# Performance work log

Hardware: AMD Instinct MI355X
Metric: run time of the kernel (lower is better)

The kernel has to match this reference:

```python
import jax, jax.numpy as jnp
import numpy as np

T, B, C = 4, 2, 128
LT, LH, LW = 8, 32, 32
NUM_HEADS = 8
HEAD_DIM = C // NUM_HEADS
THETA = 0.7
V_TH = 1.0
TAU = 2.0  # spikingjelly LIFNode default tau
N_WIN = (2, 2, 2)
TOPK = 4
EPS = 1e-5
ATAN_ALPHA = 2.0  # spikingjelly surrogate.ATan default


@jax.custom_vjp
def spike(x):
    return (x >= 0.0).astype(x.dtype)

def _spike_fwd(x):
    return spike(x), x

def _spike_bwd(x, g):
    s = (jnp.pi / 2.0) * ATAN_ALPHA * x
    return (g * (ATAN_ALPHA / 2.0) / (1.0 + s * s),)

spike.defvjp(_spike_fwd, _spike_bwd)


def lif(x_seq):
    """Multi-step LIF: v'=v+(x-v)/tau, spike at v>=V_TH, hard reset to 0 (detached)."""
    def step(v, x):
        v = v + (x - v) / TAU
        s = spike(v - V_TH)
        v = v * (1.0 - jax.lax.stop_gradient(s))  # detach_reset, v_reset=0
        return v, s
    _, s_seq = jax.lax.scan(step, jnp.zeros_like(x_seq[0]), x_seq)
    return s_seq


def bn(x, gamma, beta):
    # BatchNorm3d(track_running_stats=False) on [T*B, C, D, H, W]: batch stats per channel
    mean = x.mean(axis=(0, 1, 3, 4, 5), keepdims=True)
    var = x.var(axis=(0, 1, 3, 4, 5), keepdims=True)
    shp = (1, 1, -1, 1, 1, 1)
    return (x - mean) * jax.lax.rsqrt(var + EPS) * gamma.reshape(shp) + beta.reshape(shp)


def conv3d(x, w, pad):
    t, b = x.shape[:2]
    y = jax.lax.conv_general_dilated(
        x.reshape((t * b,) + x.shape[2:]), w,
        window_strides=(1, 1, 1), padding=[(pad, pad)] * 3,
        dimension_numbers=('NCDHW', 'OIDHW', 'NCDHW'))
    return y.reshape((t, b) + y.shape[1:])


def cdc_t(x, w):
    out = conv3d(x, w, 1)
    # central-difference temporal term: 1x1x1 conv with summed first/last temporal slices
    kd = w[:, :, 0].sum((-1, -2)) + w[:, :, 2].sum((-1, -2))  # [O, I]
    return out - THETA * jnp.einsum('oi,tbidhw->tbodhw', kd, x)


def to_wins(t):
    wt, wh, ww = N_WIN
    Tn, Bn, Cn, Lt, Lh, Lw = t.shape
    lt, lh, lw = Lt // wt, Lh // wh, Lw // ww
    t = t.reshape(Tn, Bn, Cn, wt, lt, wh, lh, ww, lw)
    t = t.transpose(0, 1, 3, 5, 7, 4, 6, 8, 2)
    return t.reshape(Tn, Bn, wt * wh * ww, lt * lh * lw, Cn)


def setup_inputs() -> dict:
    key = jax.random.key(0)
    ks = jax.random.split(key, 4)
    x = jax.random.normal(ks[0], (T, B, C, LT, LH, LW), jnp.float32)
    qw = jax.random.normal(ks[1], (C, C, 3, 3, 3), jnp.float32) / np.sqrt(C * 27)
    kw = jax.random.normal(ks[2], (C, C), jnp.float32) / np.sqrt(C)
    pw = jax.random.normal(ks[3], (C, C), jnp.float32) / np.sqrt(C)
    ones = jnp.ones((C,), jnp.float32)
    zeros = jnp.zeros((C,), jnp.float32)
    return {"x": x, "qw": qw, "q_gamma": ones, "q_beta": zeros,
            "kw": kw, "k_gamma": ones, "k_beta": zeros,
            "v_gamma": ones, "v_beta": zeros,
            "pw": pw, "p_gamma": ones, "p_beta": zeros}


def reference(x, qw, q_gamma, q_beta, kw, k_gamma, k_beta,
              v_gamma, v_beta, pw, p_gamma, p_beta):
    Tn, Bn, Cn, Lt, Lh, Lw = x.shape
    wt, wh, ww = N_WIN
    num_wins = wt * wh * ww
    lt, lh, lw = Lt // wt, Lh // wh, Lw // ww

    q_real = bn(cdc_t(x, qw), q_gamma, q_beta)
    k_real = bn(jnp.einsum('oi,tbidhw->tbodhw', kw, x), k_gamma, k_beta)

    # region-level routing from pre-spike activations
    q_region = to_wins(q_real).mean(axis=(0, 3))  # [B, W, C]
    k_region = to_wins(k_real).mean(axis=(0, 3))
    a_r = jnp.einsum('bwc,bvc->bwv', q_region, k_region) * (HEAD_DIM ** -0.5)
    k_eff = min(TOPK, num_wins)
    _, idx = jax.lax.top_k(a_r, k_eff)  # [B, W, k]

    q = lif(q_real)
    k = lif(k_real)
    v = lif(bn(x, v_gamma, v_beta))
    q_w = to_wins(q)  # [T,B,W,S,C]
    k_w = to_wins(k)
    v_w = to_wins(v)

    # gather routed windows per (batch, target window), mean-aggregate over top-k
    gather = jax.vmap(lambda src_b, idx_b: src_b[:, idx_b], in_axes=(1, 0), out_axes=1)
    k_agg = gather(k_w, idx).mean(axis=3)  # [T,B,W,S,C]
    v_agg = gather(v_w, idx).mean(axis=3)

    S = q_w.shape[3]
    q_h = q_w.reshape(Tn, Bn, num_wins, S, NUM_HEADS, HEAD_DIM)
    k_h = k_agg.reshape(Tn, Bn, num_wins, S, NUM_HEADS, HEAD_DIM)
    v_h = v_agg.reshape(Tn, Bn, num_wins, S, NUM_HEADS, HEAD_DIM)

    attn = (q_h * k_h).sum(axis=5, keepdims=True)  # [T,B,W,S,H,1]
    attn = lif(attn)
    out = (attn * v_h).reshape(Tn, Bn, num_wins, S, Cn)

    out = out.reshape(Tn, Bn, wt, wh, ww, lt, lh, lw, Cn)
    out = out.transpose(0, 1, 8, 2, 5, 3, 6, 4, 7).reshape(Tn, Bn, Cn, Lt, Lh, Lw)

    out = lif(out)
    out = bn(jnp.einsum('oi,tbidhw->tbodhw', pw, out), p_gamma, p_beta)
    return out
```

## Files before the change

### kernel.cpp

```cpp
#include <hip/hip_runtime.h>

#define TT 4
#define BB 2
#define CC 128
#define DD 8
#define HHH 32
#define WWW 32
#define PP (DD*HHH*WWW)
#define TSTRIDE (BB*CC*PP)
#define NWIN 8
#define SSS 1024
#define NHEAD 8
#define HDIM 16
#define THETA 0.7f
#define VTH 1.0f
#define NPERC (TT*BB*PP)
#define EPSf 1e-5f

typedef unsigned short ushortT;
typedef unsigned char ucharT;
typedef unsigned int uintT;
typedef _Float16 half_t;
typedef _Float16 f16x8 __attribute__((ext_vector_type(8)));
typedef float    f32x16 __attribute__((ext_vector_type(16)));

typedef const __attribute__((address_space(1))) void* as1_cvp;
typedef __attribute__((address_space(3))) void* as3_vp;

__global__ __launch_bounds__(256) void prep_wfrag(const float* __restrict__ qw,
                                                  half_t* __restrict__ wfrag) {
    int id = blockIdx.x*256 + threadIdx.x;
    if (id >= 8*27*4*64) return;
    int lane = id & 63;
    int r = id >> 6;
    int m = r & 3; r >>= 2;
    int t = r % 27;
    int kb = r / 27;
    int o   = m*32 + (lane & 31);
    int ic0 = kb*16 + (lane>>5)*8;
    size_t base = ((size_t)(id>>6))*2*64*8 + (size_t)lane*8;
    #pragma unroll
    for (int j=0;j<8;j++){
        const float* wp = qw + ((size_t)o*CC + ic0 + j)*27;
        float v = wp[t];
        if (t == 13) {
            float kd = 0.f;
            #pragma unroll
            for (int tt=0; tt<9; tt++) kd += wp[tt] + wp[18+tt];
            v -= THETA*kd;
        }
        half_t h = (half_t)v;
        half_t l = (half_t)(v - (float)h);
        wfrag[base + 0*64*8 + j] = h;
        wfrag[base + 1*64*8 + j] = l;
    }
}

__global__ __launch_bounds__(256) void prep_w1frag2(const float* __restrict__ Wk,
                                                    const float* __restrict__ Wp,
                                                    half_t* __restrict__ fragk,
                                                    half_t* __restrict__ fragp) {
    int id = blockIdx.x*256 + threadIdx.x;
    if (id >= 4096) return;
    const float* W    = (id < 2048) ? Wk : Wp;
    half_t*      frag = (id < 2048) ? fragk : fragp;
    int i2 = id & 2047;
    int lane = i2 & 63;
    int r = i2 >> 6;
    int m = r & 3;
    int kb = r >> 2;
    int o   = m*32 + (lane & 31);
    int ic0 = kb*16 + (lane>>5)*8;
    size_t base = ((size_t)(kb*4+m))*2*64*8 + (size_t)lane*8;
    #pragma unroll
    for (int j=0;j<8;j++){
        float v = W[(size_t)o*CC + ic0 + j];
        half_t h = (half_t)v;
        half_t l = (half_t)(v - (float)h);
        frag[base + 0*64*8 + j] = h;
        frag[base + 1*64*8 + j] = l;
    }
}

__global__ __launch_bounds__(256) void build_xsplit(const float* __restrict__ x,
                                                    half_t* __restrict__ xsp) {
    int id = blockIdx.x*256 + threadIdx.x;
    if (id >= 8*16*8*34*34) return;
    int wt = id % 34; int r = id/34;
    int hp = r % 34;  r /= 34;
    int dz = r % 8;   r /= 8;
    int icg = r & 15; int tb = r >> 4;
    bool inb = (hp>=1) & (hp<=32) & (wt>=1) & (wt<=32);
    half_t h8[8], l8[8];
    #pragma unroll
    for (int j=0;j<8;j++){
        float v = 0.f;
        if (inb)
            v = x[((size_t)(tb*CC + icg*8+j))*PP + (size_t)dz*1024 + (hp-1)*32 + (wt-1)];
        half_t h = (half_t)v;
        half_t l = (half_t)(v - (float)h);
        h8[j]=h; l8[j]=l;
    }
    #pragma unroll
    for (int sp=0; sp<2; sp++){
        size_t gu = (((((size_t)tb*2 + sp)*16 + icg)*8 + dz)*34 + hp)*34 + wt;
        half_t* dst = xsp + gu*8;
        const half_t* src = (sp==0)?h8:l8;
        #pragma unroll
        for (int j=0;j<8;j++) dst[j] = src[j];
    }
}

__global__ __launch_bounds__(512,2) void conv_mfma4(const half_t* __restrict__ xsp,
                                                    const half_t* __restrict__ wfrag,
                                                    float* __restrict__ y) {
    extern __shared__ half_t slab[];
    int tid  = threadIdx.x;
    int wid  = tid >> 6;
    int lane = tid & 63;
    int ln   = lane & 31;
    int half_ = lane >> 5;
    int hg = blockIdx.x;
    int dp = blockIdx.y;
    int tb = blockIdx.z;
    int H0 = hg*4, d0 = dp*2;
    int r  = wid & 3;
    int mh = wid >> 2;

    auto STAGE = [&](int kb, int bsel) {
        half_t* bufp = slab + (size_t)bsel*(3264*8);
        #pragma unroll 1
        for (int k2=0; k2<7; k2++) {
            int u = tid + (k2<<9);
            if (u < 3264) {
                int sp  = (u >= 1632) ? 1 : 0;
                int r1  = u - sp*1632;
                int icg = (r1 >= 816) ? 1 : 0;
                int p2  = r1 - icg*816;
                int dzs = p2/204; int r3 = p2 - dzs*204;
                int hp  = r3/34;  int wt = r3 - hp*34;
                int dd  = d0 - 1 + dzs;
                const half_t* src = ((unsigned)dd < 8u)
                    ? &xsp[((((((size_t)tb*2 + sp)*16 + (kb*2+icg))*8 + dd)*34 + (H0+hp))*34 + wt)*8]
                    : &xsp[(size_t)ln*8];
                __builtin_amdgcn_global_load_lds((as1_cvp)src,
                    (as3_vp)(bufp + (size_t)u*8), 16, 0, 0);
            }
        }
    };

    f32x16 accA[2][2], accB[2][2];
    #pragma unroll
    for (int dt=0;dt<2;dt++)
        #pragma unroll
        for (int mm=0;mm<2;mm++)
            #pragma unroll
            for (int i=0;i<16;i++){ accA[dt][mm][i]=0.f; accB[dt][mm][i]=0.f; }

    f16x8 ca[2][2];
    #pragma unroll
    for (int mm=0;mm<2;mm++)
        #pragma unroll
        for (int sp=0;sp<2;sp++)
            ca[mm][sp] = *(const f16x8*)&wfrag[((((size_t)0*4 + (mh*2+mm))*2+sp)*64 + lane)*8];

    asm volatile("" ::: "memory");
    STAGE(0,0);
    STAGE(1,1);
    asm volatile("" ::: "memory");

    auto KBODY = [&](int kk, f32x16 (&acc)[2][2]) {
        if (kk == 0) {
            if (wid < 3) asm volatile("s_waitcnt vmcnt(7)" ::: "memory");
            else         asm volatile("s_waitcnt vmcnt(6)" ::: "memory");
        } else {
            asm volatile("s_waitcnt vmcnt(63)" ::: "memory");
        }
        __builtin_amdgcn_s_barrier();
        asm volatile("" ::: "memory");
        const half_t* bufp = slab + (size_t)(kk&1)*(3264*8);

        f16x8 cbC[2][2], cbN[2][2];
        #pragma unroll
        for (int dt=0; dt<2; dt++){
            int unitb = dt*204 + r*34 + ln;
            #pragma unroll
            for (int sp=0; sp<2; sp++)
                cbC[dt][sp] = *(const f16x8*)&bufp[(size_t)((sp*2+half_)*816 + unitb)*8];
        }

        #pragma unroll 1
        for (int t=0; t<27; t++) {
            int t2 = (t<26)? t+1 : 26;
            int dz2=t2/9; int rr2=t2-dz2*9; int dh2=rr2/3; int dw2=rr2-dh2*3;
            #pragma unroll
            for (int dt=0; dt<2; dt++){
                int unitb = (dt + dz2)*204 + (r+dh2)*34 + (ln+dw2);
                #pragma unroll
                for (int sp=0; sp<2; sp++)
                    cbN[dt][sp] = *(const f16x8*)&bufp[(size_t)((sp*2+half_)*816 + unitb)*8];
            }
            f16x8 na[2][2];
            int nt  = (t<26)? t+1 : 0;
            int nkb = (t<26)? kk  : ((kk<7)? kk+1 : kk);
            #pragma unroll
            for (int mm=0;mm<2;mm++)
                #pragma unroll
                for (int sp=0;sp<2;sp++)
                    na[mm][sp] = *(const f16x8*)&wfrag[((((size_t)(nkb*27+nt)*4+(mh*2+mm))*2+sp)*64 + lane)*8];
            #pragma unroll
            for (int dt=0;dt<2;dt++)
                #pragma unroll
                for (int mm=0;mm<2;mm++) acc[dt][mm] = __builtin_amdgcn_mfma_f32_32x32x16_f16(ca[mm][0], cbC[dt][0], acc[dt][mm],0,0,0);
            #pragma unroll
            for (int dt=0;dt<2;dt++)
                #pragma unroll
                for (int mm=0;mm<2;mm++) acc[dt][mm] = __builtin_amdgcn_mfma_f32_32x32x16_f16(ca[mm][0], cbC[dt][1], acc[dt][mm],0,0,0);
            #pragma unroll
            for (int dt=0;dt<2;dt++)
                #pragma unroll
                for (int mm=0;mm<2;mm++) acc[dt][mm] = __builtin_amdgcn_mfma_f32_32x32x16_f16(ca[mm][1], cbC[dt][0], acc[dt][mm],0,0,0);
            #pragma unroll
            for (int dt=0;dt<2;dt++)
                #pragma unroll
                for (int sp=0;sp<2;sp++) cbC[dt][sp] = cbN[dt][sp];
            #pragma unroll
            for (int mm=0;mm<2;mm++)
                #pragma unroll
                for (int sp=0;sp<2;sp++) ca[mm][sp] = na[mm][sp];
        }
        asm volatile("" ::: "memory");
        __builtin_amdgcn_s_barrier();
        asm volatile("" ::: "memory");
        if (kk < 6) STAGE(kk+2, kk&1);
    };

    #pragma unroll 1
    for (int kk=0; kk<4; kk++) KBODY(kk, accA);
    #pragma unroll 1
    for (int kk=4; kk<8; kk++) KBODY(kk, accB);

    int h = H0 + r;
    #pragma unroll
    for (int dt=0; dt<2; dt++) {
        int d = d0 + dt;
        #pragma unroll
        for (int mm=0; mm<2; mm++) {
            #pragma unroll
            for (int reg=0; reg<16; reg++) {
                int row = (reg&3) + 8*(reg>>2) + 4*half_;
                int o = (mh*2+mm)*32 + row;
                y[((size_t)tb*CC + o)*PP + d*1024 + h*32 + ln]
                    = accA[dt][mm][reg] + accB[dt][mm][reg];
            }
        }
    }
}

__global__ __launch_bounds__(256) void kgemm_mfma(const half_t* __restrict__ xsp,
                                                  const half_t* __restrict__ wk,
                                                  float* __restrict__ y) {
    int tid  = threadIdx.x;
    int wid  = tid >> 6;
    int lane = tid & 63;
    int ln   = lane & 31;
    int half_ = lane >> 5;
    int hg = blockIdx.x, d = blockIdx.y, tb = blockIdx.z;
    int h = hg*4 + wid;

    f32x16 acc[4];
    #pragma unroll
    for (int m=0;m<4;m++)
        #pragma unroll
        for (int i=0;i<16;i++) acc[m][i] = 0.f;

    #pragma unroll 2
    for (int kb=0; kb<8; kb++) {
        f16x8 b[2];
        #pragma unroll
        for (int sp=0; sp<2; sp++) {
            size_t gu = (((((size_t)tb*2 + sp)*16 + (kb*2+half_))*8 + d)*34 + (h+1))*34 + (ln+1);
            b[sp] = *(const f16x8*)&xsp[gu*8];
        }
        #pragma unroll
        for (int m=0; m<4; m++) {
            const half_t* wb = wk + ((size_t)(kb*4+m))*2*64*8 + (size_t)lane*8;
            f16x8 a0 = *(const f16x8*)&wb[0*64*8];
            f16x8 a1 = *(const f16x8*)&wb[1*64*8];
            acc[m] = __builtin_amdgcn_mfma_f32_32x32x16_f16(a0, b[0], acc[m],0,0,0);
            acc[m] = __builtin_amdgcn_mfma_f32_32x32x16_f16(a0, b[1], acc[m],0,0,0);
            acc[m] = __builtin_amdgcn_mfma_f32_32x32x16_f16(a1, b[0], acc[m],0,0,0);
        }
    }
    #pragma unroll
    for (int m=0; m<4; m++) {
        #pragma unroll
        for (int reg=0; reg<16; reg++) {
            int row = (reg&3) + 8*(reg>>2) + 4*half_;
            int o = m*32 + row;
            y[((size_t)tb*CC + o)*PP + d*1024 + h*32 + ln] = acc[m][reg];
        }
    }
}

__global__ __launch_bounds__(256) void pgemm_mfma(const ushortT* __restrict__ spkb,
                                                  const half_t* __restrict__ wp,
                                                  float* __restrict__ y) {
    int tid  = threadIdx.x;
    int wid  = tid >> 6;
    int lane = tid & 63;
    int ln   = lane & 31;
    int half_ = lane >> 5;
    int hg = blockIdx.x, d = blockIdx.y, tb = blockIdx.z;
    int h = hg*4 + wid;
    int p = d*1024 + h*32 + ln;

    f32x16 acc[4];
    #pragma unroll
    for (int m=0;m<4;m++)
        #pragma unroll
        for (int i=0;i<16;i++) acc[m][i] = 0.f;

    #pragma unroll 2
    for (int kb=0; kb<8; kb++) {
        f16x8 b = *(const f16x8*)&spkb[(((size_t)tb*16 + (kb*2+half_))*PP + p)*8];
        #pragma unroll
        for (int m=0; m<4; m++) {
            const half_t* wb = wp + ((size_t)(kb*4+m))*2*64*8 + (size_t)lane*8;
            f16x8 a0 = *(const f16x8*)&wb[0*64*8];
            f16x8 a1 = *(const f16x8*)&wb[1*64*8];
            acc[m] = __builtin_amdgcn_mfma_f32_32x32x16_f16(a0, b, acc[m],0,0,0);
            acc[m] = __builtin_amdgcn_mfma_f32_32x32x16_f16(a1, b, acc[m],0,0,0);
        }
    }
    #pragma unroll
    for (int m=0; m<4; m++) {
        #pragma unroll
        for (int reg=0; reg<16; reg++) {
            int row = (reg&3) + 8*(reg>>2) + 4*half_;
            int o = m*32 + row;
            y[((size_t)tb*CC + o)*PP + p] = acc[m][reg];
        }
    }
}

__global__ __launch_bounds__(128) void win_stats(const float* __restrict__ q,
        const float* __restrict__ k, const float* __restrict__ x,
        float* __restrict__ rsum, float* __restrict__ rsq) {
    int blk = blockIdx.x;
    int src = blk >> 11;
    int r   = blk & 2047;
    const float* base = (src==0) ? q : ((src==1) ? k : x);
    int c  = r & 127;
    int wi = (r >> 7) & 7;
    int b  = r >> 10;
    int wd = wi>>2, wh = (wi>>1)&1, ww = wi&1;
    int tid = threadIdx.x;
    float s=0.f, s2=0.f;
    for (int t=0;t<TT;t++){
        const float* p = base + ((size_t)(t*BB+b)*CC + c)*PP;
        for (int si=tid; si<SSS; si+=128){
            int ld = si>>8, lh=(si>>4)&15, lw=si&15;
            float v = p[((wd*4+ld)<<10) + ((wh*16+lh)<<5) + (ww*16+lw)];
            s += v; s2 += v*v;
        }
    }
    __shared__ float ls[128], ls2[128];
    ls[tid]=s; ls2[tid]=s2; __syncthreads();
    for (int off=64;off>0;off>>=1){
        if(tid<off){ ls[tid]+=ls[tid+off]; ls2[tid]+=ls2[tid+off]; }
        __syncthreads();
    }
    if (tid==0){ rsum[blk]=ls[0]; rsq[blk]=ls2[0]; }
}

__global__ __launch_bounds__(384) void route_fin(const float* __restrict__ rsum,
        const float* __restrict__ rsq,
        const float* __restrict__ qg, const float* __restrict__ qb,
        const float* __restrict__ kg, const float* __restrict__ kb,
        float* __restrict__ stats, int* __restrict__ idxout) {
    __shared__ float qn[16*128], kn[16*128], ar[16*8];
    __shared__ float csum[384], csq[384];
    int tid = threadIdx.x;
    {
        int src = tid >> 7, c = tid & 127;
        float s=0.f, s2=0.f;
        for (int bw=0; bw<16; bw++){
            int idx = src*2048 + bw*128 + c;
            s  += rsum[idx];
            s2 += rsq[idx];
        }
        stats[src*256 + c]       = s;
        stats[src*256 + 128 + c] = s2;
        csum[tid]=s; csq[tid]=s2;
    }
    __syncthreads();
    for (int e=tid; e<16*128; e+=384){
        int c = e&127;
        float qm = csum[c]*(1.f/NPERC);
        float qv = csq[c]*(1.f/NPERC) - qm*qm;
        float qr = rsqrtf(qv + EPSf);
        qn[e] = (rsum[e]*(1.f/(TT*SSS)) - qm)*qr*qg[c] + qb[c];
        float km = csum[128+c]*(1.f/NPERC);
        float kv = csq[128+c]*(1.f/NPERC) - km*km;
        float kr = rsqrtf(kv + EPSf);
        kn[e] = (rsum[2048+e]*(1.f/(TT*SSS)) - km)*kr*kg[c] + kb[c];
    }
    __syncthreads();
    if (tid < 128){
        int b = tid>>6, w=(tid>>3)&7, v=tid&7;
        float s=0.f;
        for (int c=0;c<128;c++) s += qn[(b*8+w)*128+c]*kn[(b*8+v)*128+c];
        ar[(b*8+w)*8+v] = s * 0.25f;
    }
    __syncthreads();
    if (tid < 16){
        const float* row = &ar[tid*8];
        bool used[8] = {false,false,false,false,false,false,false,false};
        for (int j=0;j<4;j++){
            int best=0; float bv=-3.0e38f;
            for (int v=0; v<8; v++){
                if (!used[v] && row[v] > bv){ bv=row[v]; best=v; }
            }
            used[best]=true;
            idxout[tid*4+j]=best;
        }
    }
}

__global__ __launch_bounds__(256) void lif_bn_win3(const float* __restrict__ qin,
        const float* __restrict__ kin, const float* __restrict__ xin,
        ucharT* __restrict__ qs, ucharT* __restrict__ ks, ucharT* __restrict__ vs,
        const float* __restrict__ stats,
        const float* __restrict__ qg, const float* __restrict__ qb,
        const float* __restrict__ kg, const float* __restrict__ kb,
        const float* __restrict__ vg, const float* __restrict__ vb) {
    int src = blockIdx.y;
    const float* in  = (src==0) ? qin : ((src==1) ? kin : xin);
    ucharT*      spk = (src==0) ? qs  : ((src==1) ? ks  : vs);
    const float* gamma = (src==0) ? qg : ((src==1) ? kg : vg);
    const float* beta  = (src==0) ? qb : ((src==1) ? kb : vb);
    int e4 = blockIdx.x*256 + threadIdx.x;
    if (e4 >= BB*CC*PP/4) return;
    int e = e4*4;
    int p = e & (PP-1);
    int c = (e >> 13) & 127;
    int b = e >> 20;
    float mean = stats[src*256 + c]*(1.f/NPERC);
    float var  = stats[src*256 + 128 + c]*(1.f/NPERC) - mean*mean;
    float sc = rsqrtf(var+EPSf)*gamma[c];
    float sh = beta[c] - mean*sc;
    int d = p>>10, h=(p>>5)&31, w=p&31;
    int wi = ((d>>2)*2 + (h>>4))*2 + (w>>4);
    int si = (((d&3)<<4) + (h&15))*16 + (w&15);
    size_t widx = ((size_t)(b*NWIN+wi)*CC + c)*SSS + si;
    float v[4] = {0.f,0.f,0.f,0.f};
    #pragma unroll
    for (int t=0;t<TT;t++){
        float4 raw = *(const float4*)&in[(size_t)t*TSTRIDE + e];
        float xs[4] = {raw.x, raw.y, raw.z, raw.w};
        uintT pack = 0;
        #pragma unroll
        for (int i=0;i<4;i++){
            float xn = xs[i]*sc + sh;
            v[i] = (v[i]+xn)*0.5f;
            float s = (v[i]>=VTH)?1.f:0.f;
            pack |= (v[i]>=VTH ? 1u : 0u) << (8*i);
            v[i] *= (1.f - s);
        }
        *(uintT*)&spk[(size_t)t*TSTRIDE + widx] = pack;
    }
}

__global__ __launch_bounds__(256) void attn_lif(const ucharT* __restrict__ qspk,
        const ucharT* __restrict__ kspk, const ucharT* __restrict__ vspk,
        const int* __restrict__ idx, ushortT* __restrict__ spkb) {
    int id = blockIdx.x*256 + threadIdx.x;
    int ddq = id & 3;
    int s4  = (id>>2) & 255;
    int hh  = (id>>10) & 7;
    int wi  = (id>>13) & 7;
    int b   = id>>16;
    int bw  = b*NWIN+wi;
    int s0  = s4*4;
    int dd0 = ddq*4;
    size_t qbase = ((size_t)bw*CC + hh*HDIM + dd0)*SSS + s0;
    size_t sbase[4];
    #pragma unroll
    for (int j=0;j<4;j++){
        int srcw = idx[bw*4+j];
        sbase[j] = ((size_t)(b*NWIN+srcw)*CC + hh*HDIM + dd0)*SSS + s0;
    }
    int wd = wi>>2, wh = (wi>>1)&1, ww = wi&1;
    int d3 = wd*4 + (s0>>8), h3 = wh*16 + ((s0>>4)&15), w3 = ww*16 + (s0&15);
    int p0 = (d3<<10) + (h3<<5) + w3;
    int icg  = hh*2 + (ddq>>1);
    int slot = (ddq&1)*4;

    float v[4] = {0.f,0.f,0.f,0.f};
    float v2[4][4];
    #pragma unroll
    for (int i=0;i<4;i++)
        #pragma unroll
        for (int si=0;si<4;si++) v2[i][si]=0.f;

    #pragma unroll 1
    for (int t=0;t<TT;t++){
        size_t toff = (size_t)t*TSTRIDE;
        uintT km[4] = {0,0,0,0}, vm[4] = {0,0,0,0};
        #pragma unroll
        for (int j=0;j<4;j++){
            const ucharT* kp = kspk+toff+sbase[j];
            const ucharT* vp = vspk+toff+sbase[j];
            #pragma unroll
            for (int i=0; i<4; i++){
                km[i] += *(const uintT*)&kp[(size_t)i*SSS];
                vm[i] += *(const uintT*)&vp[(size_t)i*SSS];
            }
        }
        const ucharT* qp = qspk+toff+qbase;
        uintT atti = 0;
        #pragma unroll
        for (int i=0;i<4;i++){
            uintT q4 = *(const uintT*)&qp[(size_t)i*SSS];
            uintT tq = (q4 + 0x7F7F7F7Fu) & 0x80808080u;
            uintT mask = tq - (tq >> 7);
            atti += km[i] & mask;
        }
        atti += (uintT)__shfl_xor((int)atti, 1);
        atti += (uintT)__shfl_xor((int)atti, 2);
        int tb2 = t*BB + b;
        size_t obase = (((size_t)tb2*16 + icg)*PP + p0)*8 + slot;
        #pragma unroll
        for (int si=0; si<4; si++){
            float att = (float)((atti >> (8*si)) & 255u) * 0.25f;
            v[si] = (v[si]+att)*0.5f;
            float sp = (v[si]>=VTH)?1.f:0.f;
            v[si] *= (1.f-sp);
            float spq = sp*0.25f;
            uintT lo=0, hi=0;
            #pragma unroll
            for (int i=0;i<4;i++){
                float ov = spq*(float)((vm[i] >> (8*si)) & 255u);
                v2[i][si] = (v2[i][si]+ov)*0.5f;
                float s2 = (v2[i][si]>=VTH)?1.f:0.f;
                v2[i][si] *= (1.f-s2);
                uintT bs = (s2 != 0.f) ? 0x3C00u : 0u;
                if (i<2) lo |= bs << (16*i); else hi |= bs << (16*(i-2));
            }
            uint2 pk; pk.x = lo; pk.y = hi;
            *(uint2*)&spkb[obase + (size_t)si*8] = pk;
        }
    }
}

__global__ __launch_bounds__(256) void pstats_part(const float* __restrict__ xin,
        float* __restrict__ part_sum, float* __restrict__ part_sq) {
    int blk = blockIdx.x;
    int c = blk & 127, tb = blk >> 7;
    int tid = threadIdx.x;
    const float* p = xin + ((size_t)tb*CC + c)*PP;
    float s=0.f, s2=0.f;
    for (int i=tid; i<PP; i+=256){ float v=p[i]; s+=v; s2+=v*v; }
    __shared__ float ls[256], ls2[256];
    ls[tid]=s; ls2[tid]=s2; __syncthreads();
    for (int off=128; off>0; off>>=1){
        if (tid<off){ ls[tid]+=ls[tid+off]; ls2[tid]+=ls2[tid+off]; }
        __syncthreads();
    }
    if (tid==0){ part_sum[blk]=ls[0]; part_sq[blk]=ls2[0]; }
}

__global__ __launch_bounds__(256) void bn_apply(const float* __restrict__ xin,
        float* __restrict__ yout,
        const float* __restrict__ part_sum, const float* __restrict__ part_sq,
        const float* __restrict__ gamma, const float* __restrict__ beta) {
    size_t i = (size_t)blockIdx.x*256 + threadIdx.x;
    if (i >= (size_t)TT*BB*CC*PP) return;
    int c = (int)((i>>13)&127);
    float s=0.f, s2=0.f;
    #pragma unroll
    for (int tb=0; tb<8; tb++){
        s  += part_sum[tb*128+c];
        s2 += part_sq[tb*128+c];
    }
    float mean = s*(1.f/NPERC);
    float var  = s2*(1.f/NPERC) - mean*mean;
    float sc = rsqrtf(var+EPSf)*gamma[c];
    float sh = beta[c] - mean*sc;
    yout[i] = xin[i]*sc + sh;
}

extern "C" void kernel_launch(void* const* d_in, const int* in_sizes, int n_in,
                              void* d_out, int out_size, void* d_ws, size_t ws_size,
                              hipStream_t stream) {
    const float* x  = (const float*)d_in[0];
    const float* qw = (const float*)d_in[1];
    const float* qg = (const float*)d_in[2];
    const float* qb = (const float*)d_in[3];
    const float* kw = (const float*)d_in[4];
    const float* kg = (const float*)d_in[5];
    const float* kb = (const float*)d_in[6];
    const float* vg = (const float*)d_in[7];
    const float* vb = (const float*)d_in[8];
    const float* pw = (const float*)d_in[9];
    const float* pg = (const float*)d_in[10];
    const float* pb = (const float*)d_in[11];
    float* out = (float*)d_out;
    float* ws  = (float*)d_ws;

    const size_t NEL = (size_t)TT*TSTRIDE;
    float* qconv = ws;
    half_t* xsp  = (half_t*)(ws + 2*NEL);
    const size_t KCONV_OFF = 2*NEL + 10747904;
    float* kconv = ws + KCONV_OFF;
    float* wf_base = ws + KCONV_OFF + NEL;
    half_t* wfrag  = (half_t*)wf_base;
    half_t* wkfrag = (half_t*)(wf_base + 442368);
    half_t* wpfrag = (half_t*)(wf_base + 442368 + 16384 + 442368);
    float* stats = ws + 5*NEL;
    float* rsum = stats + 1024;
    float* rsq  = rsum + 6144;
    float* ppart_sum = rsq + 6144;
    float* ppart_sq  = ppart_sum + 1024;
    int*   idxp = (int*)(ppart_sq + 1024);

    ucharT* qspk = (ucharT*)(ws + 2*NEL);
    ucharT* kspk = (ucharT*)(ws + 2*NEL) + 8388608;
    ucharT* vspk = (ucharT*)(ws + 2*NEL) + 16777216;
    ushortT* spkb  = (ushortT*)ws;
    float*  pconv  = ws + KCONV_OFF;

    prep_wfrag<<<216,256,0,stream>>>(qw, wfrag);
    prep_w1frag2<<<16,256,0,stream>>>(kw, pw, wkfrag, wpfrag);
    build_xsplit<<<4624,256,0,stream>>>(x, xsp);
    {
        static bool attr_set = false;
        const int shmem = 2*3264*8*(int)sizeof(half_t);
        if (!attr_set) {
            hipFuncSetAttribute((const void*)conv_mfma4,
                                hipFuncAttributeMaxDynamicSharedMemorySize, shmem);
            attr_set = true;
        }
        dim3 cg(8,4,8);
        conv_mfma4<<<cg,512,shmem,stream>>>(xsp, wfrag, qconv);
    }
    {
        dim3 gg(8,8,8);
        kgemm_mfma<<<gg,256,0,stream>>>(xsp, wkfrag, kconv);
    }
    win_stats<<<6144,128,0,stream>>>(qconv, kconv, x, rsum, rsq);
    route_fin<<<1,384,0,stream>>>(rsum, rsq, qg,qb,kg,kb, stats, idxp);
    {
        dim3 lg(2048,3);
        lif_bn_win3<<<lg,256,0,stream>>>(qconv,kconv,x,
                                         qspk,kspk,vspk,
                                         stats, qg,qb,kg,kb,vg,vb);
    }
    attn_lif<<<512,256,0,stream>>>(qspk,kspk,vspk,idxp,spkb);
    {
        dim3 gg(8,8,8);
        pgemm_mfma<<<gg,256,0,stream>>>(spkb, wpfrag, pconv);
    }
    pstats_part<<<1024,256,0,stream>>>(pconv, ppart_sum, ppart_sq);
    bn_apply<<<32768,256,0,stream>>>(pconv, out, ppart_sum, ppart_sq, pg, pb);
}
```

Before: 385.8 us.

## Fuse prep kernels, merge k-GEMM into conv, fold BN stats into p-GEMM

Combines the three preparation kernels into one launch and runs the 1x1 k-projection GEMM inside the 3x3x3 conv kernel after its main loop. The projection GEMM now accumulates per-channel sum and sum-of-squares through shared-memory and global atomics, which removes the separate statistics pass; the accumulators are zeroed inside attn_lif. bn_apply reads the totals directly and uses float4 vector loads and stores. This cuts launch count and one full read of the projection output, at the cost of atomic contention, a longer conv kernel tail, and atomic-order nondeterminism in the BN statistics.

```diff
diff --git a/kernel.cpp b/kernel.cpp
--- a/kernel.cpp
+++ b/kernel.cpp
@@ -27,93 +27,97 @@
 typedef const __attribute__((address_space(1))) void* as1_cvp;
 typedef __attribute__((address_space(3))) void* as3_vp;
 
-__global__ __launch_bounds__(256) void prep_wfrag(const float* __restrict__ qw,
-                                                  half_t* __restrict__ wfrag) {
-    int id = blockIdx.x*256 + threadIdx.x;
-    if (id >= 8*27*4*64) return;
-    int lane = id & 63;
-    int r = id >> 6;
-    int m = r & 3; r >>= 2;
-    int t = r % 27;
-    int kb = r / 27;
-    int o   = m*32 + (lane & 31);
-    int ic0 = kb*16 + (lane>>5)*8;
-    size_t base = ((size_t)(id>>6))*2*64*8 + (size_t)lane*8;
-    #pragma unroll
-    for (int j=0;j<8;j++){
-        const float* wp = qw + ((size_t)o*CC + ic0 + j)*27;
-        float v = wp[t];
-        if (t == 13) {
-            float kd = 0.f;
-            #pragma unroll
-            for (int tt=0; tt<9; tt++) kd += wp[tt] + wp[18+tt];
-            v -= THETA*kd;
-        }
-        half_t h = (half_t)v;
-        half_t l = (half_t)(v - (float)h);
-        wfrag[base + 0*64*8 + j] = h;
-        wfrag[base + 1*64*8 + j] = l;
-    }
-}
-
-__global__ __launch_bounds__(256) void prep_w1frag2(const float* __restrict__ Wk,
-                                                    const float* __restrict__ Wp,
-                                                    half_t* __restrict__ fragk,
-                                                    half_t* __restrict__ fragp) {
-    int id = blockIdx.x*256 + threadIdx.x;
-    if (id >= 4096) return;
-    const float* W    = (id < 2048) ? Wk : Wp;
-    half_t*      frag = (id < 2048) ? fragk : fragp;
-    int i2 = id & 2047;
-    int lane = i2 & 63;
-    int r = i2 >> 6;
-    int m = r & 3;
-    int kb = r >> 2;
-    int o   = m*32 + (lane & 31);
-    int ic0 = kb*16 + (lane>>5)*8;
-    size_t base = ((size_t)(kb*4+m))*2*64*8 + (size_t)lane*8;
-    #pragma unroll
-    for (int j=0;j<8;j++){
-        float v = W[(size_t)o*CC + ic0 + j];
-        half_t h = (half_t)v;
-        half_t l = (half_t)(v - (float)h);
-        frag[base + 0*64*8 + j] = h;
-        frag[base + 1*64*8 + j] = l;
-    }
-}
-
-__global__ __launch_bounds__(256) void build_xsplit(const float* __restrict__ x,
-                                                    half_t* __restrict__ xsp) {
-    int id = blockIdx.x*256 + threadIdx.x;
-    if (id >= 8*16*8*34*34) return;
-    int wt = id % 34; int r = id/34;
-    int hp = r % 34;  r /= 34;
-    int dz = r % 8;   r /= 8;
-    int icg = r & 15; int tb = r >> 4;
-    bool inb = (hp>=1) & (hp<=32) & (wt>=1) & (wt<=32);
-    half_t h8[8], l8[8];
-    #pragma unroll
-    for (int j=0;j<8;j++){
-        float v = 0.f;
-        if (inb)
-            v = x[((size_t)(tb*CC + icg*8+j))*PP + (size_t)dz*1024 + (hp-1)*32 + (wt-1)];
-        half_t h = (half_t)v;
-        half_t l = (half_t)(v - (float)h);
-        h8[j]=h; l8[j]=l;
-    }
-    #pragma unroll
-    for (int sp=0; sp<2; sp++){
-        size_t gu = (((((size_t)tb*2 + sp)*16 + icg)*8 + dz)*34 + hp)*34 + wt;
-        half_t* dst = xsp + gu*8;
-        const half_t* src = (sp==0)?h8:l8;
-        #pragma unroll
-        for (int j=0;j<8;j++) dst[j] = src[j];
+__global__ __launch_bounds__(256) void prep_all(const float* __restrict__ qw,
+                                                const float* __restrict__ Wk,
+                                                const float* __restrict__ Wp,
+                                                const float* __restrict__ x,
+                                                half_t* __restrict__ wfrag,
+                                                half_t* __restrict__ fragk,
+                                                half_t* __restrict__ fragp,
+                                                half_t* __restrict__ xsp) {
+    int bid = blockIdx.x;
+    int tid = threadIdx.x;
+    if (bid < 216) {
+        int id = bid*256 + tid;
+        if (id >= 8*27*4*64) return;
+        int lane = id & 63;
+        int r = id >> 6;
+        int m = r & 3; r >>= 2;
+        int t = r % 27;
+        int kb = r / 27;
+        int o   = m*32 + (lane & 31);
+        int ic0 = kb*16 + (lane>>5)*8;
+        size_t base = ((size_t)(id>>6))*2*64*8 + (size_t)lane*8;
+        #pragma unroll
+        for (int j=0;j<8;j++){
+            const float* wp = qw + ((size_t)o*CC + ic0 + j)*27;
+            float v = wp[t];
+            if (t == 13) {
+                float kd = 0.f;
+                #pragma unroll
+                for (int tt=0; tt<9; tt++) kd += wp[tt] + wp[18+tt];
+                v -= THETA*kd;
+            }
+            half_t h = (half_t)v;
+            half_t l = (half_t)(v - (float)h);
+            wfrag[base + 0*64*8 + j] = h;
+            wfrag[base + 1*64*8 + j] = l;
+        }
+    } else if (bid < 232) {
+        int id = (bid-216)*256 + tid;
+        if (id >= 4096) return;
+        const float* W    = (id < 2048) ? Wk : Wp;
+        half_t*      frag = (id < 2048) ? fragk : fragp;
+        int i2 = id & 2047;
+        int lane = i2 & 63;
+        int r = i2 >> 6;
+        int m = r & 3;
+        int kb = r >> 2;
+        int o   = m*32 + (lane & 31);
+        int ic0 = kb*16 + (lane>>5)*8;
+        size_t base = ((size_t)(kb*4+m))*2*64*8 + (size_t)lane*8;
+        #pragma unroll
+        for (int j=0;j<8;j++){
+            float v = W[(size_t)o*CC + ic0 + j];
+            half_t h = (half_t)v;
+            half_t l = (half_t)(v - (float)h);
+            frag[base + 0*64*8 + j] = h;
+            frag[base + 1*64*8 + j] = l;
+        }
+    } else {
+        int id = (bid-232)*256 + tid;
+        if (id >= 8*16*8*34*34) return;
+        int wt = id % 34; int r = id/34;
+        int hp = r % 34;  r /= 34;
+        int dz = r % 8;   r /= 8;
+        int icg = r & 15; int tb = r >> 4;
+        bool inb = (hp>=1) & (hp<=32) & (wt>=1) & (wt<=32);
+        half_t h8[8], l8[8];
+        #pragma unroll
+        for (int j=0;j<8;j++){
+            float v = 0.f;
+            if (inb)
+                v = x[((size_t)(tb*CC + icg*8+j))*PP + (size_t)dz*1024 + (hp-1)*32 + (wt-1)];
+            half_t h = (half_t)v;
+            half_t l = (half_t)(v - (float)h);
+            h8[j]=h; l8[j]=l;
+        }
+        #pragma unroll
+        for (int sp=0; sp<2; sp++){
+            size_t gu = (((((size_t)tb*2 + sp)*16 + icg)*8 + dz)*34 + hp)*34 + wt;
+            half_t* dst = xsp + gu*8;
+            const half_t* src = (sp==0)?h8:l8;
+            #pragma unroll
+            for (int j=0;j<8;j++) dst[j] = src[j];
+        }
     }
 }
 
 __global__ __launch_bounds__(512,2) void conv_mfma4(const half_t* __restrict__ xsp,
                                                     const half_t* __restrict__ wfrag,
-                                                    float* __restrict__ y) {
+                                                    const half_t* __restrict__ wk,
+                                                    float* __restrict__ y,
+                                                    float* __restrict__ yk) {
     extern __shared__ half_t slab[];
     int tid  = threadIdx.x;
     int wid  = tid >> 6;
@@ -240,72 +244,69 @@
     #pragma unroll 1
     for (int kk=4; kk<8; kk++) KBODY(kk, accB);
 
-    int h = H0 + r;
-    #pragma unroll
-    for (int dt=0; dt<2; dt++) {
-        int d = d0 + dt;
-        #pragma unroll
-        for (int mm=0; mm<2; mm++) {
+    {
+        int h = H0 + r;
+        #pragma unroll
+        for (int dt=0; dt<2; dt++) {
+            int d = d0 + dt;
+            #pragma unroll
+            for (int mm=0; mm<2; mm++) {
+                #pragma unroll
+                for (int reg=0; reg<16; reg++) {
+                    int row = (reg&3) + 8*(reg>>2) + 4*half_;
+                    int o = (mh*2+mm)*32 + row;
+                    y[((size_t)tb*CC + o)*PP + d*1024 + h*32 + ln]
+                        = accA[dt][mm][reg] + accB[dt][mm][reg];
+                }
+            }
+        }
+    }
+
+    {
+        int d = d0 + (wid >> 2);
+        int h = H0 + (wid & 3);
+        f32x16 kacc[4];
+        #pragma unroll
+        for (int m=0;m<4;m++)
+            #pragma unroll
+            for (int i=0;i<16;i++) kacc[m][i] = 0.f;
+
+        #pragma unroll 2
+        for (int kb=0; kb<8; kb++) {
+            f16x8 b[2];
+            #pragma unroll
+            for (int sp=0; sp<2; sp++) {
+                size_t gu = (((((size_t)tb*2 + sp)*16 + (kb*2+half_))*8 + d)*34 + (h+1))*34 + (ln+1);
+                b[sp] = *(const f16x8*)&xsp[gu*8];
+            }
+            #pragma unroll
+            for (int m=0; m<4; m++) {
+                const half_t* wb = wk + ((size_t)(kb*4+m))*2*64*8 + (size_t)lane*8;
+                f16x8 a0 = *(const f16x8*)&wb[0*64*8];
+                f16x8 a1 = *(const f16x8*)&wb[1*64*8];
+                kacc[m] = __builtin_amdgcn_mfma_f32_32x32x16_f16(a0, b[0], kacc[m],0,0,0);
+                kacc[m] = __builtin_amdgcn_mfma_f32_32x32x16_f16(a0, b[1], kacc[m],0,0,0);
+                kacc[m] = __builtin_amdgcn_mfma_f32_32x32x16_f16(a1, b[0], kacc[m],0,0,0);
+            }
+        }
+        #pragma unroll
+        for (int m=0; m<4; m++) {
             #pragma unroll
             for (int reg=0; reg<16; reg++) {
                 int row = (reg&3) + 8*(reg>>2) + 4*half_;
-                int o = (mh*2+mm)*32 + row;
-                y[((size_t)tb*CC + o)*PP + d*1024 + h*32 + ln]
-                    = accA[dt][mm][reg] + accB[dt][mm][reg];
-            }
-        }
-    }
-}
-
-__global__ __launch_bounds__(256) void kgemm_mfma(const half_t* __restrict__ xsp,
-                                                  const half_t* __restrict__ wk,
-                                                  float* __restrict__ y) {
-    int tid  = threadIdx.x;
-    int wid  = tid >> 6;
-    int lane = tid & 63;
-    int ln   = lane & 31;
-    int half_ = lane >> 5;
-    int hg = blockIdx.x, d = blockIdx.y, tb = blockIdx.z;
-    int h = hg*4 + wid;
-
-    f32x16 acc[4];
-    #pragma unroll
-    for (int m=0;m<4;m++)
-        #pragma unroll
-        for (int i=0;i<16;i++) acc[m][i] = 0.f;
-
-    #pragma unroll 2
-    for (int kb=0; kb<8; kb++) {
-        f16x8 b[2];
-        #pragma unroll
-        for (int sp=0; sp<2; sp++) {
-            size_t gu = (((((size_t)tb*2 + sp)*16 + (kb*2+half_))*8 + d)*34 + (h+1))*34 + (ln+1);
-            b[sp] = *(const f16x8*)&xsp[gu*8];
-        }
-        #pragma unroll
-        for (int m=0; m<4; m++) {
-            const half_t* wb = wk + ((size_t)(kb*4+m))*2*64*8 + (size_t)lane*8;
-            f16x8 a0 = *(const f16x8*)&wb[0*64*8];
-            f16x8 a1 = *(const f16x8*)&wb[1*64*8];
-            acc[m] = __builtin_amdgcn_mfma_f32_32x32x16_f16(a0, b[0], acc[m],0,0,0);
-            acc[m] = __builtin_amdgcn_mfma_f32_32x32x16_f16(a0, b[1], acc[m],0,0,0);
-            acc[m] = __builtin_amdgcn_mfma_f32_32x32x16_f16(a1, b[0], acc[m],0,0,0);
-        }
-    }
-    #pragma unroll
-    for (int m=0; m<4; m++) {
-        #pragma unroll
-        for (int reg=0; reg<16; reg++) {
-            int row = (reg&3) + 8*(reg>>2) + 4*half_;
-            int o = m*32 + row;
-            y[((size_t)tb*CC + o)*PP + d*1024 + h*32 + ln] = acc[m][reg];
+                int o = m*32 + row;
+                yk[((size_t)tb*CC + o)*PP + d*1024 + h*32 + ln] = kacc[m][reg];
+            }
         }
     }
 }
 
 __global__ __launch_bounds__(256) void pgemm_mfma(const ushortT* __restrict__ spkb,
                                                   const half_t* __restrict__ wp,
-                                                  float* __restrict__ y) {
+                                                  float* __restrict__ y,
+                                                  float* __restrict__ psum,
+                                                  float* __restrict__ psq) {
+    __shared__ float ls[128], ls2[128];
     int tid  = threadIdx.x;
     int wid  = tid >> 6;
     int lane = tid & 63;
@@ -314,6 +315,8 @@
     int hg = blockIdx.x, d = blockIdx.y, tb = blockIdx.z;
     int h = hg*4 + wid;
     int p = d*1024 + h*32 + ln;
+    if (tid < 128){ ls[tid]=0.f; ls2[tid]=0.f; }
+    __syncthreads();
 
     f32x16 acc[4];
     #pragma unroll
@@ -339,8 +342,16 @@
         for (int reg=0; reg<16; reg++) {
             int row = (reg&3) + 8*(reg>>2) + 4*half_;
             int o = m*32 + row;
-            y[((size_t)tb*CC + o)*PP + p] = acc[m][reg];
-        }
+            float v = acc[m][reg];
+            y[((size_t)tb*CC + o)*PP + p] = v;
+            atomicAdd(&ls[o], v);
+            atomicAdd(&ls2[o], v*v);
+        }
+    }
+    __syncthreads();
+    if (tid < 128){
+        atomicAdd(&psum[tid], ls[tid]);
+        atomicAdd(&psq[tid],  ls2[tid]);
     }
 }
 
@@ -474,7 +485,9 @@
 
 __global__ __launch_bounds__(256) void attn_lif(const ucharT* __restrict__ qspk,
         const ucharT* __restrict__ kspk, const ucharT* __restrict__ vspk,
-        const int* __restrict__ idx, ushortT* __restrict__ spkb) {
+        const int* __restrict__ idx, ushortT* __restrict__ spkb,
+        float* __restrict__ pz) {
+    if (blockIdx.x == 0 && threadIdx.x < 256) pz[threadIdx.x] = 0.f;
     int id = blockIdx.x*256 + threadIdx.x;
     int ddq = id & 3;
     int s4  = (id>>2) & 255;
@@ -554,41 +567,24 @@
     }
 }
 
-__global__ __launch_bounds__(256) void pstats_part(const float* __restrict__ xin,
-        float* __restrict__ part_sum, float* __restrict__ part_sq) {
-    int blk = blockIdx.x;
-    int c = blk & 127, tb = blk >> 7;
-    int tid = threadIdx.x;
-    const float* p = xin + ((size_t)tb*CC + c)*PP;
-    float s=0.f, s2=0.f;
-    for (int i=tid; i<PP; i+=256){ float v=p[i]; s+=v; s2+=v*v; }
-    __shared__ float ls[256], ls2[256];
-    ls[tid]=s; ls2[tid]=s2; __syncthreads();
-    for (int off=128; off>0; off>>=1){
-        if (tid<off){ ls[tid]+=ls[tid+off]; ls2[tid]+=ls2[tid+off]; }
-        __syncthreads();
-    }
-    if (tid==0){ part_sum[blk]=ls[0]; part_sq[blk]=ls2[0]; }
-}
-
 __global__ __launch_bounds__(256) void bn_apply(const float* __restrict__ xin,
         float* __restrict__ yout,
-        const float* __restrict__ part_sum, const float* __restrict__ part_sq,
+        const float* __restrict__ sum, const float* __restrict__ sq,
         const float* __restrict__ gamma, const float* __restrict__ beta) {
-    size_t i = (size_t)blockIdx.x*256 + threadIdx.x;
-    if (i >= (size_t)TT*BB*CC*PP) return;
+    size_t i4 = (size_t)blockIdx.x*256 + threadIdx.x;
+    if (i4 >= (size_t)TT*BB*CC*PP/4) return;
+    size_t i = i4*4;
     int c = (int)((i>>13)&127);
-    float s=0.f, s2=0.f;
-    #pragma unroll
-    for (int tb=0; tb<8; tb++){
-        s  += part_sum[tb*128+c];
-        s2 += part_sq[tb*128+c];
-    }
-    float mean = s*(1.f/NPERC);
-    float var  = s2*(1.f/NPERC) - mean*mean;
+    float mean = sum[c]*(1.f/NPERC);
+    float var  = sq[c]*(1.f/NPERC) - mean*mean;
     float sc = rsqrtf(var+EPSf)*gamma[c];
     float sh = beta[c] - mean*sc;
-    yout[i] = xin[i]*sc + sh;
+    float4 a = *(const float4*)&xin[i];
+    a.x = a.x*sc + sh;
+    a.y = a.y*sc + sh;
+    a.z = a.z*sc + sh;
+    a.w = a.w*sc + sh;
+    *(float4*)&yout[i] = a;
 }
 
 extern "C" void kernel_launch(void* const* d_in, const int* in_sizes, int n_in,
@@ -621,9 +617,9 @@
     float* stats = ws + 5*NEL;
     float* rsum = stats + 1024;
     float* rsq  = rsum + 6144;
-    float* ppart_sum = rsq + 6144;
-    float* ppart_sq  = ppart_sum + 1024;
-    int*   idxp = (int*)(ppart_sq + 1024);
+    float* psum = rsq + 6144;
+    float* psq  = psum + 128;
+    int*   idxp = (int*)(psq + 128);
 
     ucharT* qspk = (ucharT*)(ws + 2*NEL);
     ucharT* kspk = (ucharT*)(ws + 2*NEL) + 8388608;
@@ -631,9 +627,7 @@
     ushortT* spkb  = (ushortT*)ws;
     float*  pconv  = ws + KCONV_OFF;
 
-    prep_wfrag<<<216,256,0,stream>>>(qw, wfrag);
-    prep_w1frag2<<<16,256,0,stream>>>(kw, pw, wkfrag, wpfrag);
-    build_xsplit<<<4624,256,0,stream>>>(x, xsp);
+    prep_all<<<4856,256,0,stream>>>(qw, kw, pw, x, wfrag, wkfrag, wpfrag, xsp);
     {
         static bool attr_set = false;
         const int shmem = 2*3264*8*(int)sizeof(half_t);
@@ -643,11 +637,7 @@
             attr_set = true;
         }
         dim3 cg(8,4,8);
-        conv_mfma4<<<cg,512,shmem,stream>>>(xsp, wfrag, qconv);
-    }
-    {
-        dim3 gg(8,8,8);
-        kgemm_mfma<<<gg,256,0,stream>>>(xsp, wkfrag, kconv);
+        conv_mfma4<<<cg,512,shmem,stream>>>(xsp, wfrag, wkfrag, qconv, kconv);
     }
     win_stats<<<6144,128,0,stream>>>(qconv, kconv, x, rsum, rsq);
     route_fin<<<1,384,0,stream>>>(rsum, rsq, qg,qb,kg,kb, stats, idxp);
@@ -657,11 +647,10 @@
                                          qspk,kspk,vspk,
                                          stats, qg,qb,kg,kb,vg,vb);
     }
-    attn_lif<<<512,256,0,stream>>>(qspk,kspk,vspk,idxp,spkb);
+    attn_lif<<<512,256,0,stream>>>(qspk,kspk,vspk,idxp,spkb,psum);
     {
         dim3 gg(8,8,8);
-        pgemm_mfma<<<gg,256,0,stream>>>(spkb, wpfrag, pconv);
-    }
-    pstats_part<<<1024,256,0,stream>>>(pconv, ppart_sum, ppart_sq);
-    bn_apply<<<32768,256,0,stream>>>(pconv, out, ppart_sum, ppart_sq, pg, pb);
-}
+        pgemm_mfma<<<gg,256,0,stream>>>(spkb, wpfrag, pconv, psum, psq);
+    }
+    bn_apply<<<8192,256,0,stream>>>(pconv, out, psum, psq, pg, pb);
+}
```

After: 461.1 us. 1.2x slower.
